# Optimization experiments

Hardware: AMD Instinct MI355X
Metric: run time of the kernel (lower is better)

The kernel has to match this reference:

```python
import jax, jax.numpy as jnp
import numpy as np

B, T, I, H, P = 256, 2048, 2, 128, 129  # batch, max_len, input feats, hidden, num_pitches


def setup_inputs() -> dict:
    key = jax.random.key(0)
    ks = jax.random.split(key, 8)
    s = 1.0 / np.sqrt(H)  # torch LSTM/Linear init scale
    x = jax.random.normal(ks[0], (B, T, I), jnp.float32)
    lengths = jax.random.randint(ks[1], (B,), 1, T + 1, jnp.int32)
    W_ih = jax.random.uniform(ks[2], (4 * H, I), jnp.float32, -s, s)
    W_hh = jax.random.uniform(ks[3], (4 * H, H), jnp.float32, -s, s)
    note_W = jax.random.uniform(ks[4], (P, H), jnp.float32, -s, s)
    note_b = jax.random.uniform(ks[5], (P,), jnp.float32, -s, s)
    dur_W = jax.random.uniform(ks[6], (1, H), jnp.float32, -s, s)
    dur_b = jax.random.uniform(ks[7], (1,), jnp.float32, -s, s)
    return dict(x=x, lengths=lengths, W_ih=W_ih, W_hh=W_hh,
                note_W=note_W, note_b=note_b, dur_W=dur_W, dur_b=dur_b)


def _lstm(x, lengths, W_ih, W_hh):
    # Precompute input projections for all timesteps in one GEMM: [T,B,4H]
    pre = jnp.einsum('bti,gi->tbg', x, W_ih)
    h0 = jnp.zeros((x.shape[0], W_hh.shape[1]), x.dtype)
    c0 = h0
    ts = jnp.arange(x.shape[1])

    def step(carry, inp):
        h, c = carry
        px, t = inp
        gates = px + h @ W_hh.T  # [B,4H], torch gate order: i,f,g,o
        i_g, f_g, g_g, o_g = jnp.split(gates, 4, axis=-1)
        i_g = jax.nn.sigmoid(i_g)
        f_g = jax.nn.sigmoid(f_g)
        o_g = jax.nn.sigmoid(o_g)
        g_g = jnp.tanh(g_g)
        c_new = f_g * c + i_g * g_g
        h_new = o_g * jnp.tanh(c_new)
        m = (t < lengths)[:, None]  # packed semantics: freeze past length
        h2 = jnp.where(m, h_new, h)
        c2 = jnp.where(m, c_new, c)
        return (h2, c2), jnp.where(m, h_new, 0.0)

    (hT, cT), hs = jax.lax.scan(step, (h0, c0), (pre, ts))
    return jnp.transpose(hs, (1, 0, 2)), hT, cT  # [B,T,H], final states = states at last valid step


def reference(x, lengths, W_ih, W_hh, note_W, note_b, dur_W, dur_b):
    hs, hT, cT = _lstm(x, lengths, W_ih, W_hh)
    mask = (jnp.arange(x.shape[1])[None, :] < lengths[:, None])[..., None]
    note_logits = jnp.where(mask, hs @ note_W.T + note_b, 0.0)     # [B,T,129]
    duration_pred = jnp.where(mask, hs @ dur_W.T + dur_b, 0.0)     # [B,T,1]
    return note_logits, duration_pred, hT, cT
```

## Files before the change

kernel.cpp:

```cpp
#include <hip/hip_runtime.h>


typedef _Float16 f16;
typedef _Float16 f16x8 __attribute__((ext_vector_type(8)));
typedef float    f32x4 __attribute__((ext_vector_type(4)));

#define B_  256
#define T_  2048
#define H_  128
#define P_  129

static constexpr size_t NOTE_N   = (size_t)B_ * T_ * P_;
static constexpr size_t DUR_BASE = NOTE_N;
static constexpr size_t HT_BASE  = DUR_BASE + (size_t)B_ * T_;
static constexpr size_t CT_BASE  = HT_BASE + (size_t)B_ * H_;

#if defined(__has_builtin)
#if __has_builtin(__builtin_amdgcn_exp2f)
#define EXP2F(x) __builtin_amdgcn_exp2f(x)
#endif
#endif
#ifndef EXP2F
#define EXP2F(x) __expf((x) * 0.6931471805599453f)
#endif

__device__ __forceinline__ float fast_rcp(float x) { return __builtin_amdgcn_rcpf(x); }

__device__ __forceinline__ float sigmoid_f(float x) {
    float e = EXP2F(-1.44269504f * x);
    return fast_rcp(1.f + e);
}
__device__ __forceinline__ float tanh_f(float x) {
    float e = EXP2F(2.885390082f * x);
    return (e - 1.f) * fast_rcp(e + 1.f);
}

__device__ __forceinline__ f16* hs_row(float* out, int bt) {
    size_t byteoff = ((size_t)bt * (P_ * 4) + 15) & ~(size_t)15;
    return (f16*)((char*)out + byteoff);
}

__global__ __launch_bounds__(256) void prep_k(const float* __restrict__ note_W,
                                              const float* __restrict__ dur_W,
                                              f16* __restrict__ Wn) {
    int i = threadIdx.x + blockIdx.x * 256;
    if (i >= 144 * 128) return;
    int row = i >> 7, k = i & 127;
    float v = 0.f;
    if (row < 129)       v = note_W[row * 128 + k];
    else if (row == 129) v = dur_W[k];
    Wn[i] = (f16)v;
}

__global__ __launch_bounds__(512, 2) void lstm3_k(const float* __restrict__ x,
                                                  const int* __restrict__ lengths,
                                                  const float* __restrict__ W_ih,
                                                  const float* __restrict__ W_hh,
                                                  float* __restrict__ out) {
    __shared__ __align__(16) f16 h_sh[2][H_];
    __shared__ __align__(8) float2 xs[128];

    const int tid = threadIdx.x;
    const int b = blockIdx.x;
    const int w = tid >> 6;
    const int l = tid & 63;
    const int p = l & 15;
    const int q = l >> 4;
    const int j = 16 * w + p;

    f16x8 Bf[4][4];
    float wxx[4], wxy[4];
#pragma unroll
    for (int tt = 0; tt < 4; tt++) {
        const int c = j + 128 * tt;
        const float* wr = W_hh + (size_t)c * H_ + 8 * q;
#pragma unroll
        for (int kt = 0; kt < 4; kt++) {
            float4 v1 = *(const float4*)(wr + 32 * kt);
            float4 v2 = *(const float4*)(wr + 32 * kt + 4);
            f16x8 f;
            f[0] = (f16)v1.x; f[1] = (f16)v1.y; f[2] = (f16)v1.z; f[3] = (f16)v1.w;
            f[4] = (f16)v2.x; f[5] = (f16)v2.y; f[6] = (f16)v2.z; f[7] = (f16)v2.w;
            Bf[tt][kt] = f;
        }
        wxx[tt] = W_ih[2 * c];
        wxy[tt] = W_ih[2 * c + 1];
    }
    const int len = lengths[b];
    if (tid < 2 * H_) ((f16*)h_sh)[tid] = (f16)0.f;

    float c_reg = 0.f, h_reg = 0.f;
    __syncthreads();

    for (int t = 0; t < len; t++) {
        if ((t & 127) == 0) {
            if (tid < 128)
                xs[tid] = *(const float2*)(x + (size_t)b * T_ * 2 + (size_t)(t + tid) * 2);
            __syncthreads();
        }
        const int cur = t & 1;

        f16x8 Af[4];
#pragma unroll
        for (int kt = 0; kt < 4; kt++)
            Af[kt] = *(const f16x8*)(&h_sh[cur][32 * kt + 8 * q]);

        f32x4 acc[4];
#pragma unroll
        for (int tt = 0; tt < 4; tt++) acc[tt] = f32x4{0.f, 0.f, 0.f, 0.f};
#pragma unroll
        for (int kt = 0; kt < 4; kt++) {
#pragma unroll
            for (int tt = 0; tt < 4; tt++)
                acc[tt] = __builtin_amdgcn_mfma_f32_16x16x32_f16(
                    Af[kt], Bf[tt][kt], acc[tt], 0, 0, 0);
        }

        const float2 xv = xs[t & 127];
        float g0 = acc[0][0] + __builtin_fmaf(wxy[0], xv.y, wxx[0] * xv.x);
        float g1 = acc[1][0] + __builtin_fmaf(wxy[1], xv.y, wxx[1] * xv.x);
        float g2 = acc[2][0] + __builtin_fmaf(wxy[2], xv.y, wxx[2] * xv.x);
        float g3 = acc[3][0] + __builtin_fmaf(wxy[3], xv.y, wxx[3] * xv.x);

        const float ig = sigmoid_f(g0);
        const float fg = sigmoid_f(g1);
        const float gg = tanh_f(g2);
        const float og = sigmoid_f(g3);
        c_reg = __builtin_fmaf(fg, c_reg, ig * gg);
        h_reg = og * tanh_f(fminf(fmaxf(c_reg, -15.f), 15.f));

        if (q == 0) {
            const f16 h16 = (f16)h_reg;
            h_sh[cur ^ 1][j] = h16;
            hs_row(out, b * T_ + t)[j] = h16;
        }
        asm volatile("s_waitcnt lgkmcnt(0)" ::: "memory");
        __builtin_amdgcn_sched_barrier(0);
        __builtin_amdgcn_s_barrier();
        __builtin_amdgcn_sched_barrier(0);
    }

    if (q == 0) {
        out[HT_BASE + (size_t)b * H_ + j] = h_reg;
        out[CT_BASE + (size_t)b * H_ + j] = c_reg;
    }
}

__global__ __launch_bounds__(256) void proj_k(const int* __restrict__ lengths,
                                              const f16* __restrict__ Wn,
                                              const float* __restrict__ note_b,
                                              const float* __restrict__ dur_b,
                                              float* __restrict__ out) {
    __shared__ __align__(16) f16 wn_sh[144 * 136];

    const int tid = threadIdx.x;
    {
        unsigned int* dst = (unsigned int*)wn_sh;
        const unsigned int* src = (const unsigned int*)Wn;
        for (int w = tid; w < 144 * 64; w += 256) {
            int row = w >> 6, cw = w & 63;
            dst[row * 68 + cw] = src[w];
        }
    }
    __syncthreads();

    const int wv = tid >> 6;
    const int l = tid & 63;
    const int tile = blockIdx.x * 4 + wv;
    const int bt0 = tile * 16;
    const int b = bt0 >> 11;
    const int t0 = bt0 & 2047;
    const int len = lengths[b];
    const int r16 = l & 15, q = l >> 4;

    f32x4 acc[9];
#pragma unroll
    for (int nf = 0; nf < 9; nf++) acc[nf] = f32x4{0.f, 0.f, 0.f, 0.f};

    const bool live = (t0 < len);
    if (live) {
        f16x8 a[4];
        {
            const f16* ar = hs_row(out, bt0 + r16);
#pragma unroll
            for (int kk = 0; kk < 4; kk++)
                a[kk] = *(const f16x8*)(ar + kk * 32 + q * 8);
        }
#pragma unroll
        for (int nf = 0; nf < 9; nf++) {
            const f16* brow = wn_sh + (nf * 16 + r16) * 136 + q * 8;
#pragma unroll
            for (int kk = 0; kk < 4; kk++) {
                f16x8 bb = *(const f16x8*)(brow + kk * 32);
                acc[nf] = __builtin_amdgcn_mfma_f32_16x16x32_f16(a[kk], bb, acc[nf], 0, 0, 0);
            }
        }
    }

#pragma unroll
    for (int nf = 0; nf < 9; nf++) {
        int col = nf * 16 + r16;
        float bias = 0.f;
        if (col < 129)       bias = note_b[col];
        else if (col == 129) bias = dur_b[0];
#pragma unroll
        for (int r = 0; r < 4; r++) {
            int rowbt = bt0 + q * 4 + r;
            int t = t0 + q * 4 + r;
            float v = (t < len) ? (acc[nf][r] + bias) : 0.f;
            if (col < 129)
                out[(size_t)rowbt * P_ + col] = v;
            else if (col == 129)
                out[DUR_BASE + rowbt] = v;
        }
    }
}

extern "C" void kernel_launch(void* const* d_in, const int* in_sizes, int n_in,
                              void* d_out, int out_size, void* d_ws, size_t ws_size,
                              hipStream_t stream) {
    const float* x       = (const float*)d_in[0];
    const int*   lengths = (const int*)d_in[1];
    const float* W_ih    = (const float*)d_in[2];
    const float* W_hh    = (const float*)d_in[3];
    const float* note_W  = (const float*)d_in[4];
    const float* note_b  = (const float*)d_in[5];
    const float* dur_W   = (const float*)d_in[6];
    const float* dur_b   = (const float*)d_in[7];
    float* out = (float*)d_out;
    f16* Wn = (f16*)d_ws;

    prep_k<<<72, 256, 0, stream>>>(note_W, dur_W, Wn);
    lstm3_k<<<B_, 512, 0, stream>>>(x, lengths, W_ih, W_hh, out);
    proj_k<<<(B_ * T_) / 64, 256, 0, stream>>>(lengths, Wn, note_b, dur_b, out);
}
```

Measured before the change: 1.066 ms.

## Halve LSTM recurrence block to four waves, each computing eight gate tiles

The recurrent kernel now runs with 256 threads per batch row instead of 512. Each wave issues eight MFMA tiles per K step instead of four, and lanes pick their gates by quadrant. The MFMA work per SIMD stays the same, while the per-step barrier spans fewer waves and the activation work is less duplicated. The hs output address also moves from a per-step multiply and round to an incremental pointer that adds the 16-byte alignment pad every fourth step. The cost is higher register pressure from 32 B fragments, and a longer MFMA chain per wave on the serial critical path.

```diff
diff --git a/kernel.cpp b/kernel.cpp
--- a/kernel.cpp
+++ b/kernel.cpp
@@ -52,7 +52,7 @@
     Wn[i] = (f16)v;
 }
 
-__global__ __launch_bounds__(512, 2) void lstm3_k(const float* __restrict__ x,
+__global__ __launch_bounds__(256, 1) void lstm4_k(const float* __restrict__ x,
                                                   const int* __restrict__ lengths,
                                                   const float* __restrict__ W_ih,
                                                   const float* __restrict__ W_hh,
@@ -66,13 +66,15 @@
     const int l = tid & 63;
     const int p = l & 15;
     const int q = l >> 4;
-    const int j = 16 * w + p;
-
-    f16x8 Bf[4][4];
-    float wxx[4], wxy[4];
-#pragma unroll
-    for (int tt = 0; tt < 4; tt++) {
-        const int c = j + 128 * tt;
+    const int sel = q >> 1;
+    const int j = 16 * w + 64 * sel + p;
+    const bool writer = ((q & 1) == 0);
+
+    f16x8 Bf[8][4];
+    float wxx[8], wxy[8];
+#pragma unroll
+    for (int s = 0; s < 8; s++) {
+        const int c = 16 * (w + 4 * s) + p;
         const float* wr = W_hh + (size_t)c * H_ + 8 * q;
 #pragma unroll
         for (int kt = 0; kt < 4; kt++) {
@@ -81,19 +83,21 @@
             f16x8 f;
             f[0] = (f16)v1.x; f[1] = (f16)v1.y; f[2] = (f16)v1.z; f[3] = (f16)v1.w;
             f[4] = (f16)v2.x; f[5] = (f16)v2.y; f[6] = (f16)v2.z; f[7] = (f16)v2.w;
-            Bf[tt][kt] = f;
-        }
-        wxx[tt] = W_ih[2 * c];
-        wxy[tt] = W_ih[2 * c + 1];
+            Bf[s][kt] = f;
+        }
+        wxx[s] = W_ih[2 * c];
+        wxy[s] = W_ih[2 * c + 1];
     }
     const int len = lengths[b];
     if (tid < 2 * H_) ((f16*)h_sh)[tid] = (f16)0.f;
 
+    char* hp = (char*)out + (size_t)b * (T_ * 516ULL) + 2 * j;
+
     float c_reg = 0.f, h_reg = 0.f;
-    __syncthreads();
 
     for (int t = 0; t < len; t++) {
         if ((t & 127) == 0) {
+            __syncthreads();
             if (tid < 128)
                 xs[tid] = *(const float2*)(x + (size_t)b * T_ * 2 + (size_t)(t + tid) * 2);
             __syncthreads();
@@ -105,42 +109,46 @@
         for (int kt = 0; kt < 4; kt++)
             Af[kt] = *(const f16x8*)(&h_sh[cur][32 * kt + 8 * q]);
 
-        f32x4 acc[4];
-#pragma unroll
-        for (int tt = 0; tt < 4; tt++) acc[tt] = f32x4{0.f, 0.f, 0.f, 0.f};
+        f32x4 acc[8];
+#pragma unroll
+        for (int s = 0; s < 8; s++) acc[s] = f32x4{0.f, 0.f, 0.f, 0.f};
 #pragma unroll
         for (int kt = 0; kt < 4; kt++) {
 #pragma unroll
-            for (int tt = 0; tt < 4; tt++)
-                acc[tt] = __builtin_amdgcn_mfma_f32_16x16x32_f16(
-                    Af[kt], Bf[tt][kt], acc[tt], 0, 0, 0);
+            for (int s = 0; s < 8; s++)
+                acc[s] = __builtin_amdgcn_mfma_f32_16x16x32_f16(
+                    Af[kt], Bf[s][kt], acc[s], 0, 0, 0);
         }
 
         const float2 xv = xs[t & 127];
-        float g0 = acc[0][0] + __builtin_fmaf(wxy[0], xv.y, wxx[0] * xv.x);
-        float g1 = acc[1][0] + __builtin_fmaf(wxy[1], xv.y, wxx[1] * xv.x);
-        float g2 = acc[2][0] + __builtin_fmaf(wxy[2], xv.y, wxx[2] * xv.x);
-        float g3 = acc[3][0] + __builtin_fmaf(wxy[3], xv.y, wxx[3] * xv.x);
-
-        const float ig = sigmoid_f(g0);
-        const float fg = sigmoid_f(g1);
-        const float gg = tanh_f(g2);
-        const float og = sigmoid_f(g3);
+        float G[4];
+#pragma unroll
+        for (int tt = 0; tt < 4; tt++) {
+            const int s = sel + 2 * tt;
+            G[tt] = acc[s][0] + __builtin_fmaf(wxy[s], xv.y, wxx[s] * xv.x);
+        }
+
+        const float ig = sigmoid_f(G[0]);
+        const float fg = sigmoid_f(G[1]);
+        const float gg = tanh_f(G[2]);
+        const float og = sigmoid_f(G[3]);
         c_reg = __builtin_fmaf(fg, c_reg, ig * gg);
         h_reg = og * tanh_f(fminf(fmaxf(c_reg, -15.f), 15.f));
 
-        if (q == 0) {
+        if (writer) {
             const f16 h16 = (f16)h_reg;
             h_sh[cur ^ 1][j] = h16;
-            hs_row(out, b * T_ + t)[j] = h16;
-        }
+            *(f16*)hp = h16;
+        }
+        hp += 512 + (((t & 3) == 0) ? 16 : 0);
+
         asm volatile("s_waitcnt lgkmcnt(0)" ::: "memory");
         __builtin_amdgcn_sched_barrier(0);
         __builtin_amdgcn_s_barrier();
         __builtin_amdgcn_sched_barrier(0);
     }
 
-    if (q == 0) {
+    if (writer) {
         out[HT_BASE + (size_t)b * H_ + j] = h_reg;
         out[CT_BASE + (size_t)b * H_ + j] = c_reg;
     }
@@ -231,6 +239,6 @@
     f16* Wn = (f16*)d_ws;
 
     prep_k<<<72, 256, 0, stream>>>(note_W, dur_W, Wn);
-    lstm3_k<<<B_, 512, 0, stream>>>(x, lengths, W_ih, W_hh, out);
+    lstm4_k<<<B_, 256, 0, stream>>>(x, lengths, W_ih, W_hh, out);
     proj_k<<<(B_ * T_) / 64, 256, 0, stream>>>(lengths, Wn, note_b, dur_b, out);
 }
```

Measured after the change: 2.384 ms. +123.5%, slower.

## Batch 16 sequences per LSTM block to fill all MFMA rows

Applied to the files above, without the earlier changes.

The recurrent kernel now processes 16 batch sequences per workgroup, so each of the 16 MFMA rows carries a different sequence's hidden state instead of 16 copies of one. Each lane applies the gate update for 4 sequences, with per-sequence length masking. Stores to the hs buffer use incremental pointers that reproduce the padded row alignment. The grid shrinks from 256 blocks to 16. Each block now loops to the longest of its 16 lengths, and per-step elementwise and transcendental work per lane grows fourfold, which may lengthen the serial critical path.

```diff
diff --git a/kernel.cpp b/kernel.cpp
--- a/kernel.cpp
+++ b/kernel.cpp
@@ -9,6 +9,7 @@
 #define T_  2048
 #define H_  128
 #define P_  129
+#define NB  16
 
 static constexpr size_t NOTE_N   = (size_t)B_ * T_ * P_;
 static constexpr size_t DUR_BASE = NOTE_N;
@@ -52,21 +53,22 @@
     Wn[i] = (f16)v;
 }
 
-__global__ __launch_bounds__(512, 2) void lstm3_k(const float* __restrict__ x,
+__global__ __launch_bounds__(512, 2) void lstm5_k(const float* __restrict__ x,
                                                   const int* __restrict__ lengths,
                                                   const float* __restrict__ W_ih,
                                                   const float* __restrict__ W_hh,
                                                   float* __restrict__ out) {
-    __shared__ __align__(16) f16 h_sh[2][H_];
-    __shared__ __align__(8) float2 xs[128];
+    __shared__ __align__(16) f16   h_sh[2][NB][136];
+    __shared__ __align__(16) float xs[64][NB][2];
 
     const int tid = threadIdx.x;
-    const int b = blockIdx.x;
-    const int w = tid >> 6;
-    const int l = tid & 63;
-    const int p = l & 15;
-    const int q = l >> 4;
-    const int j = 16 * w + p;
+    const int g   = blockIdx.x;
+    const int bg  = g * NB;
+    const int w   = tid >> 6;
+    const int l   = tid & 63;
+    const int p   = l & 15;
+    const int q   = l >> 4;
+    const int j   = 16 * w + p;
 
     f16x8 Bf[4][4];
     float wxx[4], wxy[4];
@@ -86,64 +88,93 @@
         wxx[tt] = W_ih[2 * c];
         wxy[tt] = W_ih[2 * c + 1];
     }
-    const int len = lengths[b];
-    if (tid < 2 * H_) ((f16*)h_sh)[tid] = (f16)0.f;
-
-    float c_reg = 0.f, h_reg = 0.f;
-    __syncthreads();
-
-    for (int t = 0; t < len; t++) {
-        if ((t & 127) == 0) {
-            if (tid < 128)
-                xs[tid] = *(const float2*)(x + (size_t)b * T_ * 2 + (size_t)(t + tid) * 2);
+
+    const int len0 = lengths[bg + 4 * q + 0];
+    const int len1 = lengths[bg + 4 * q + 1];
+    const int len2 = lengths[bg + 4 * q + 2];
+    const int len3 = lengths[bg + 4 * q + 3];
+    int maxlen = 0;
+    for (int k = 0; k < NB; k++) maxlen = max(maxlen, lengths[bg + k]);
+
+    for (int i = tid; i < 2 * NB * 136; i += 512) ((f16*)h_sh)[i] = (f16)0.f;
+
+    char* hp0 = (char*)out + (size_t)(bg + 4 * q + 0) * (T_ * 516ULL) + 2 * j;
+    char* hp1 = (char*)out + (size_t)(bg + 4 * q + 1) * (T_ * 516ULL) + 2 * j;
+    char* hp2 = (char*)out + (size_t)(bg + 4 * q + 2) * (T_ * 516ULL) + 2 * j;
+    char* hp3 = (char*)out + (size_t)(bg + 4 * q + 3) * (T_ * 516ULL) + 2 * j;
+
+    const f32x4 z4 = {0.f, 0.f, 0.f, 0.f};
+    float c0 = 0.f, c1 = 0.f, c2 = 0.f, c3 = 0.f;
+    float h0 = 0.f, h1 = 0.f, h2 = 0.f, h3 = 0.f;
+
+    for (int t = 0; t < maxlen; t++) {
+        if ((t & 63) == 0) {
+            const int b = tid & 15, tp = tid >> 4;
+            float4 v = *(const float4*)(x + (size_t)(bg + b) * (T_ * 2)
+                                          + (size_t)(t + 2 * tp) * 2);
+            *(float2*)&xs[2 * tp][b][0]     = make_float2(v.x, v.y);
+            *(float2*)&xs[2 * tp + 1][b][0] = make_float2(v.z, v.w);
             __syncthreads();
         }
         const int cur = t & 1;
+        const int nxt = cur ^ 1;
 
         f16x8 Af[4];
 #pragma unroll
         for (int kt = 0; kt < 4; kt++)
-            Af[kt] = *(const f16x8*)(&h_sh[cur][32 * kt + 8 * q]);
+            Af[kt] = *(const f16x8*)(&h_sh[cur][p][32 * kt + 8 * q]);
+
+        const float4 xq0 = *(const float4*)(&xs[t & 63][4 * q][0]);
+        const float4 xq1 = *(const float4*)(&xs[t & 63][4 * q + 2][0]);
 
         f32x4 acc[4];
 #pragma unroll
-        for (int tt = 0; tt < 4; tt++) acc[tt] = f32x4{0.f, 0.f, 0.f, 0.f};
-#pragma unroll
-        for (int kt = 0; kt < 4; kt++) {
+        for (int tt = 0; tt < 4; tt++)
+            acc[tt] = __builtin_amdgcn_mfma_f32_16x16x32_f16(Af[0], Bf[tt][0], z4, 0, 0, 0);
+#pragma unroll
+        for (int kt = 1; kt < 4; kt++) {
 #pragma unroll
             for (int tt = 0; tt < 4; tt++)
                 acc[tt] = __builtin_amdgcn_mfma_f32_16x16x32_f16(
                     Af[kt], Bf[tt][kt], acc[tt], 0, 0, 0);
         }
 
-        const float2 xv = xs[t & 127];
-        float g0 = acc[0][0] + __builtin_fmaf(wxy[0], xv.y, wxx[0] * xv.x);
-        float g1 = acc[1][0] + __builtin_fmaf(wxy[1], xv.y, wxx[1] * xv.x);
-        float g2 = acc[2][0] + __builtin_fmaf(wxy[2], xv.y, wxx[2] * xv.x);
-        float g3 = acc[3][0] + __builtin_fmaf(wxy[3], xv.y, wxx[3] * xv.x);
-
-        const float ig = sigmoid_f(g0);
-        const float fg = sigmoid_f(g1);
-        const float gg = tanh_f(g2);
-        const float og = sigmoid_f(g3);
-        c_reg = __builtin_fmaf(fg, c_reg, ig * gg);
-        h_reg = og * tanh_f(fminf(fmaxf(c_reg, -15.f), 15.f));
-
-        if (q == 0) {
-            const f16 h16 = (f16)h_reg;
-            h_sh[cur ^ 1][j] = h16;
-            hs_row(out, b * T_ + t)[j] = h16;
-        }
+#define UPDATE(R, XVX, XVY, CV, HV, LEN, HP) {                                   \
+        float G0 = acc[0][R] + __builtin_fmaf(wxy[0], XVY, wxx[0] * (XVX));      \
+        float G1 = acc[1][R] + __builtin_fmaf(wxy[1], XVY, wxx[1] * (XVX));      \
+        float G2 = acc[2][R] + __builtin_fmaf(wxy[2], XVY, wxx[2] * (XVX));      \
+        float G3 = acc[3][R] + __builtin_fmaf(wxy[3], XVY, wxx[3] * (XVX));      \
+        float ig = sigmoid_f(G0), fg = sigmoid_f(G1);                            \
+        float gg = tanh_f(G2),    og = sigmoid_f(G3);                            \
+        float cn = __builtin_fmaf(fg, CV, ig * gg);                              \
+        float hn = og * tanh_f(fminf(fmaxf(cn, -15.f), 15.f));                   \
+        bool m = (t < LEN);                                                      \
+        CV = m ? cn : CV;  HV = m ? hn : HV;                                     \
+        f16 h16 = (f16)HV;                                                       \
+        h_sh[nxt][4 * q + R][j] = h16;                                           \
+        if (m) *(f16*)HP = h16;                                                  \
+        HP += 512 + (((t & 3) == 0) ? 16 : 0);                                   \
+    }
+        UPDATE(0, xq0.x, xq0.y, c0, h0, len0, hp0)
+        UPDATE(1, xq0.z, xq0.w, c1, h1, len1, hp1)
+        UPDATE(2, xq1.x, xq1.y, c2, h2, len2, hp2)
+        UPDATE(3, xq1.z, xq1.w, c3, h3, len3, hp3)
+#undef UPDATE
+
         asm volatile("s_waitcnt lgkmcnt(0)" ::: "memory");
         __builtin_amdgcn_sched_barrier(0);
         __builtin_amdgcn_s_barrier();
         __builtin_amdgcn_sched_barrier(0);
     }
 
-    if (q == 0) {
-        out[HT_BASE + (size_t)b * H_ + j] = h_reg;
-        out[CT_BASE + (size_t)b * H_ + j] = c_reg;
-    }
+    out[HT_BASE + (size_t)(bg + 4 * q + 0) * H_ + j] = h0;
+    out[HT_BASE + (size_t)(bg + 4 * q + 1) * H_ + j] = h1;
+    out[HT_BASE + (size_t)(bg + 4 * q + 2) * H_ + j] = h2;
+    out[HT_BASE + (size_t)(bg + 4 * q + 3) * H_ + j] = h3;
+    out[CT_BASE + (size_t)(bg + 4 * q + 0) * H_ + j] = c0;
+    out[CT_BASE + (size_t)(bg + 4 * q + 1) * H_ + j] = c1;
+    out[CT_BASE + (size_t)(bg + 4 * q + 2) * H_ + j] = c2;
+    out[CT_BASE + (size_t)(bg + 4 * q + 3) * H_ + j] = c3;
 }
 
 __global__ __launch_bounds__(256) void proj_k(const int* __restrict__ lengths,
@@ -231,6 +262,6 @@
     f16* Wn = (f16*)d_ws;
 
     prep_k<<<72, 256, 0, stream>>>(note_W, dur_W, Wn);
-    lstm3_k<<<B_, 512, 0, stream>>>(x, lengths, W_ih, W_hh, out);
+    lstm5_k<<<B_ / NB, 512, 0, stream>>>(x, lengths, W_ih, W_hh, out);
     proj_k<<<(B_ * T_) / 64, 256, 0, stream>>>(lengths, Wn, note_b, dur_b, out);
 }
```

After: 2.373 ms. 123% more time.
